# Kernel tuning notes

Hardware: AMD Instinct MI355X
Metric: run time of the kernel (lower is better)

The kernel has to match this reference:

```python
import jax, jax.numpy as jnp
import numpy as np

P, B, I, O = 32, 512, 1024, 1024


def setup_inputs() -> dict:
    key = jax.random.key(0)
    kx, kw = jax.random.split(key)
    # strictly {0,1}-valued binary tensors stored as float32, as in the torch module
    x = (jax.random.uniform(kx, (P, B, I)) > 0.5).astype(jnp.float32)
    w = (jax.random.uniform(kw, (2, P, I, O)) > 0.5).astype(jnp.float32)
    return {"x": x, "w": w}


def reference(x, w):
    # x: [P, B, I] binary; w: [2, P, I, O] binary.
    # out = x @ W0 + (~x) @ W1  (logical_not of a {0,1} float is 1 - x)
    notx = 1.0 - x
    out = jnp.einsum('pbi,pio->pbo', x, w[0]) + jnp.einsum('pbi,pio->pbo', notx, w[1])
    return out  # [P, B, O], activation == 'none'
```

## Files before the change

kernel.cpp:

```cpp
#include <hip/hip_runtime.h>


namespace {

constexpr int PP = 32;
constexpr int BB = 512;
constexpr int II = 1024;
constexpr int OO = 1024;

typedef __attribute__((ext_vector_type(8))) short bf16x8;
typedef __attribute__((ext_vector_type(4))) float f32x4;

__device__ __forceinline__ unsigned pk2(float lo, float hi) {
    return (__float_as_uint(lo) >> 16) | (__float_as_uint(hi) & 0xFFFF0000u);
}

__global__ __launch_bounds__(256, 2) void ebl_prep(const float* __restrict__ x,
                                                   const float* __restrict__ w,
                                                   unsigned short* __restrict__ dWT,
                                                   unsigned short* __restrict__ xbf,
                                                   float* __restrict__ colsum) {
    const int t = (int)threadIdx.x;
    const int bid = (int)blockIdx.x;

    if (bid < 256) {
        const int p  = bid >> 3;
        const int o0 = (bid & 7) * 128;
        const int og = t & 31;
        const int kg = t >> 5;
        const int o  = o0 + 4 * og;
        const float* w0p = w + (size_t)p * (II * OO) + o;
        const float* w1p = w + (size_t)(PP + p) * (II * OO) + o;

        float cs0 = 0.f, cs1 = 0.f, cs2 = 0.f, cs3 = 0.f;

        for (int it = 0; it < 16; ++it) {
            const int kb = 64 * it + 8 * kg;
            const float* r0 = w0p + (size_t)kb * OO;
            const float* r1 = w1p + (size_t)kb * OO;
            f32x4 q0[8], q1[8];
#pragma unroll
            for (int j = 0; j < 8; ++j) q0[j] = *(const f32x4*)(r0 + (size_t)j * OO);
#pragma unroll
            for (int j = 0; j < 8; ++j) q1[j] = *(const f32x4*)(r1 + (size_t)j * OO);

#pragma unroll
            for (int c = 0; c < 4; ++c) {
                uint4 st;
                st.x = pk2(q0[0][c] - q1[0][c], q0[1][c] - q1[1][c]);
                st.y = pk2(q0[2][c] - q1[2][c], q0[3][c] - q1[3][c]);
                st.z = pk2(q0[4][c] - q1[4][c], q0[5][c] - q1[5][c]);
                st.w = pk2(q0[6][c] - q1[6][c], q0[7][c] - q1[7][c]);
                *(uint4*)(&dWT[((size_t)p * OO + o + c) * II + kb]) = st;
            }
#pragma unroll
            for (int j = 0; j < 8; ++j) {
                cs0 += q1[j].x; cs1 += q1[j].y; cs2 += q1[j].z; cs3 += q1[j].w;
            }
        }

        __shared__ float Scr[8 * 128];
        *(f32x4*)(&Scr[kg * 128 + 4 * og]) = (f32x4){cs0, cs1, cs2, cs3};
        __syncthreads();
        if (t < 128) {
            float s = 0.f;
#pragma unroll
            for (int g = 0; g < 8; ++g) s += Scr[g * 128 + t];
            colsum[p * OO + o0 + t] = s;
        }
    } else {
        const size_t base = (size_t)(bid - 256) * 65536;
        for (int it = 0; it < 16; ++it) {
#pragma unroll
            for (int j = 0; j < 4; ++j) {
                const size_t idx = base + (size_t)it * 4096 + j * 1024 + 4 * t;
                f32x4 v = *(const f32x4*)(x + idx);
                *(uint2*)(&xbf[idx]) = make_uint2(pk2(v.x, v.y), pk2(v.z, v.w));
            }
        }
    }
}

__device__ __forceinline__ void load_lds16(const unsigned short* g, unsigned short* l) {
    __builtin_amdgcn_global_load_lds(
        (const __attribute__((address_space(1))) unsigned int*)g,
        (__attribute__((address_space(3))) unsigned int*)l, 16, 0, 0);
}

__global__ __launch_bounds__(256, 3) void ebl_gemm(const unsigned short* __restrict__ xbf,
                                                   const unsigned short* __restrict__ dWT,
                                                   const float* __restrict__ colsum,
                                                   float* __restrict__ out) {
    __shared__ __align__(16) unsigned short As[128 * 64];
    __shared__ __align__(16) unsigned short Bs[128 * 64];

    const int t  = (int)threadIdx.x;
    const int l  = t & 63;
    const int wv = t >> 6;
    const int wm = wv & 1;
    const int wn = wv >> 1;
    const int lq = l >> 4;
    const int ln = l & 15;

    const int p  = (int)blockIdx.z;
    const int b0 = (int)blockIdx.y * 128;
    const int o0 = (int)blockIdx.x * 128;

    const unsigned short* Ag = xbf + ((size_t)p * BB + b0) * II;
    const unsigned short* Bg = dWT + ((size_t)p * OO + o0) * II;

    const int ri = l >> 3, sj = l & 7;
    int gof[4], lbase[4];
#pragma unroll
    for (int q = 0; q < 4; ++q) {
        const int r0  = 8 * (4 * wv + q);
        const int row = r0 + ri;
        gof[q]   = row * II + 8 * (sj ^ (row & 7));
        lbase[q] = r0 * 64;
    }

    int aoff[2][4], boff[2][4];
#pragma unroll
    for (int s = 0; s < 2; ++s)
#pragma unroll
        for (int mt = 0; mt < 4; ++mt) {
            const int j = 8 * ((4 * s + lq) ^ (ln & 7));
            aoff[s][mt] = (wm * 64 + mt * 16 + ln) * 64 + j;
            boff[s][mt] = (wn * 64 + mt * 16 + ln) * 64 + j;
        }

    f32x4 acc[4][4];
#pragma unroll
    for (int mt = 0; mt < 4; ++mt)
#pragma unroll
        for (int nt = 0; nt < 4; ++nt)
            acc[mt][nt] = (f32x4){0.f, 0.f, 0.f, 0.f};

    for (int kk = 0; kk < II; kk += 64) {
#pragma unroll
        for (int q = 0; q < 4; ++q) {
            load_lds16(Ag + gof[q] + kk, As + lbase[q]);
            load_lds16(Bg + gof[q] + kk, Bs + lbase[q]);
        }
        __syncthreads();

#pragma unroll
        for (int s = 0; s < 2; ++s) {
            bf16x8 af[4], bfv[4];
#pragma unroll
            for (int mt = 0; mt < 4; ++mt) af[mt] = *(const bf16x8*)(As + aoff[s][mt]);
#pragma unroll
            for (int nt = 0; nt < 4; ++nt) bfv[nt] = *(const bf16x8*)(Bs + boff[s][nt]);
#pragma unroll
            for (int mt = 0; mt < 4; ++mt)
#pragma unroll
                for (int nt = 0; nt < 4; ++nt)
                    acc[mt][nt] = __builtin_amdgcn_mfma_f32_16x16x32_bf16(
                        af[mt], bfv[nt], acc[mt][nt], 0, 0, 0);
        }
        __syncthreads();
    }

    float cs[4];
#pragma unroll
    for (int nt = 0; nt < 4; ++nt)
        cs[nt] = colsum[p * OO + o0 + wn * 64 + nt * 16 + ln];

    float* op = out + ((size_t)p * BB + b0) * OO + o0;
#pragma unroll
    for (int nt = 0; nt < 4; ++nt) {
        const int ocol = wn * 64 + nt * 16 + ln;
#pragma unroll
        for (int mt = 0; mt < 4; ++mt) {
            const int row = wm * 64 + mt * 16 + lq * 4;
#pragma unroll
            for (int r = 0; r < 4; ++r)
                op[(size_t)(row + r) * OO + ocol] = acc[mt][nt][r] + cs[nt];
        }
    }
}

}

extern "C" void kernel_launch(void* const* d_in, const int* in_sizes, int n_in,
                              void* d_out, int out_size, void* d_ws, size_t ws_size,
                              hipStream_t stream) {
    const float* x = (const float*)d_in[0];
    const float* w = (const float*)d_in[1];
    float* out = (float*)d_out;

    unsigned short* dWT = (unsigned short*)d_ws;
    unsigned short* xbf = (unsigned short*)((char*)d_ws + (64u << 20));
    float* colsum = (float*)((char*)d_ws + (96u << 20));

    ebl_prep<<<dim3(512, 1, 1), dim3(256, 1, 1), 0, stream>>>(x, w, dWT, xbf, colsum);
    ebl_gemm<<<dim3(OO / 128, BB / 128, PP), dim3(256, 1, 1), 0, stream>>>(
        xbf, dWT, colsum, out);
}
```

Baseline: 483.4 us.

## Fuse fp32-to-bf16 conversion and weight differencing into a single GEMM kernel

Replaces the separate prep kernel and bf16 GEMM with one kernel. It DMAs fp32 x, W0 and W1 tiles straight into LDS, converts x to bf16 and builds (W0-W1) in bf16 in LDS, and accumulates the W1 column sums in the same pass. The colsum bias is added through an LDS-staged, vectorized output store. This drops the intermediate workspace writes and the extra launch. In exchange each block re-reads fp32 inputs across tiles (twice the bytes of bf16, redundant across output tiles), uses a smaller per-wave MFMA tile, and adds LDS conversion passes with extra barriers in every k-step.

```diff
diff --git a/kernel.cpp b/kernel.cpp
--- a/kernel.cpp
+++ b/kernel.cpp
@@ -4,7 +4,7 @@
 namespace {
 
 constexpr int PP = 32;
-constexpr int BB = 512;
+constexpr int BBATCH = 512;
 constexpr int II = 1024;
 constexpr int OO = 1024;
 
@@ -15,84 +15,25 @@
     return (__float_as_uint(lo) >> 16) | (__float_as_uint(hi) & 0xFFFF0000u);
 }
 
-__global__ __launch_bounds__(256, 2) void ebl_prep(const float* __restrict__ x,
-                                                   const float* __restrict__ w,
-                                                   unsigned short* __restrict__ dWT,
-                                                   unsigned short* __restrict__ xbf,
-                                                   float* __restrict__ colsum) {
-    const int t = (int)threadIdx.x;
-    const int bid = (int)blockIdx.x;
-
-    if (bid < 256) {
-        const int p  = bid >> 3;
-        const int o0 = (bid & 7) * 128;
-        const int og = t & 31;
-        const int kg = t >> 5;
-        const int o  = o0 + 4 * og;
-        const float* w0p = w + (size_t)p * (II * OO) + o;
-        const float* w1p = w + (size_t)(PP + p) * (II * OO) + o;
-
-        float cs0 = 0.f, cs1 = 0.f, cs2 = 0.f, cs3 = 0.f;
-
-        for (int it = 0; it < 16; ++it) {
-            const int kb = 64 * it + 8 * kg;
-            const float* r0 = w0p + (size_t)kb * OO;
-            const float* r1 = w1p + (size_t)kb * OO;
-            f32x4 q0[8], q1[8];
-#pragma unroll
-            for (int j = 0; j < 8; ++j) q0[j] = *(const f32x4*)(r0 + (size_t)j * OO);
-#pragma unroll
-            for (int j = 0; j < 8; ++j) q1[j] = *(const f32x4*)(r1 + (size_t)j * OO);
-
-#pragma unroll
-            for (int c = 0; c < 4; ++c) {
-                uint4 st;
-                st.x = pk2(q0[0][c] - q1[0][c], q0[1][c] - q1[1][c]);
-                st.y = pk2(q0[2][c] - q1[2][c], q0[3][c] - q1[3][c]);
-                st.z = pk2(q0[4][c] - q1[4][c], q0[5][c] - q1[5][c]);
-                st.w = pk2(q0[6][c] - q1[6][c], q0[7][c] - q1[7][c]);
-                *(uint4*)(&dWT[((size_t)p * OO + o + c) * II + kb]) = st;
-            }
-#pragma unroll
-            for (int j = 0; j < 8; ++j) {
-                cs0 += q1[j].x; cs1 += q1[j].y; cs2 += q1[j].z; cs3 += q1[j].w;
-            }
-        }
-
-        __shared__ float Scr[8 * 128];
-        *(f32x4*)(&Scr[kg * 128 + 4 * og]) = (f32x4){cs0, cs1, cs2, cs3};
-        __syncthreads();
-        if (t < 128) {
-            float s = 0.f;
-#pragma unroll
-            for (int g = 0; g < 8; ++g) s += Scr[g * 128 + t];
-            colsum[p * OO + o0 + t] = s;
-        }
-    } else {
-        const size_t base = (size_t)(bid - 256) * 65536;
-        for (int it = 0; it < 16; ++it) {
-#pragma unroll
-            for (int j = 0; j < 4; ++j) {
-                const size_t idx = base + (size_t)it * 4096 + j * 1024 + 4 * t;
-                f32x4 v = *(const f32x4*)(x + idx);
-                *(uint2*)(&xbf[idx]) = make_uint2(pk2(v.x, v.y), pk2(v.z, v.w));
-            }
-        }
-    }
-}
-
-__device__ __forceinline__ void load_lds16(const unsigned short* g, unsigned short* l) {
+__device__ __forceinline__ void dma16(const float* g, char* l) {
     __builtin_amdgcn_global_load_lds(
         (const __attribute__((address_space(1))) unsigned int*)g,
         (__attribute__((address_space(3))) unsigned int*)l, 16, 0, 0);
 }
 
-__global__ __launch_bounds__(256, 3) void ebl_gemm(const unsigned short* __restrict__ xbf,
-                                                   const unsigned short* __restrict__ dWT,
-                                                   const float* __restrict__ colsum,
-                                                   float* __restrict__ out) {
-    __shared__ __align__(16) unsigned short As[128 * 64];
-    __shared__ __align__(16) unsigned short Bs[128 * 64];
+constexpr int XF   = 0;
+constexpr int W0F  = 16384;
+constexpr int W1F  = 32768;
+constexpr int ABo  = 49152;
+constexpr int BBo  = 59392;
+constexpr int LDST = 69632;
+constexpr int OUTS = 0;
+constexpr int CSP  = 36864;
+
+__global__ __launch_bounds__(512, 4) void ebl_kernel(const float* __restrict__ x,
+                                                     const float* __restrict__ w,
+                                                     float* __restrict__ out) {
+    __shared__ __align__(16) char smem[LDST];
 
     const int t  = (int)threadIdx.x;
     const int l  = t & 63;
@@ -106,76 +47,153 @@
     const int b0 = (int)blockIdx.y * 128;
     const int o0 = (int)blockIdx.x * 128;
 
-    const unsigned short* Ag = xbf + ((size_t)p * BB + b0) * II;
-    const unsigned short* Bg = dWT + ((size_t)p * OO + o0) * II;
-
-    const int ri = l >> 3, sj = l & 7;
-    int gof[4], lbase[4];
-#pragma unroll
-    for (int q = 0; q < 4; ++q) {
-        const int r0  = 8 * (4 * wv + q);
-        const int row = r0 + ri;
-        gof[q]   = row * II + 8 * (sj ^ (row & 7));
-        lbase[q] = r0 * 64;
+    const float* xg  = x + ((size_t)p * BBATCH + b0) * II;
+    const float* w0g = w + (size_t)p * II * OO + o0;
+    const float* w1g = w + (size_t)(PP + p) * II * OO + o0;
+
+    const int xrow_l = (l >> 3);
+    const int xcol_l = (l & 7) * 4;
+    const int wrow_l = (l >> 5);
+    const int wcol_l = (l & 31) * 4;
+
+    int a_off[4], b_off[2];
+#pragma unroll
+    for (int mt = 0; mt < 4; ++mt)
+        a_off[mt] = ABo + (wm * 64 + mt * 16 + ln) * 80 + lq * 16;
+#pragma unroll
+    for (int nt = 0; nt < 2; ++nt)
+        b_off[nt] = BBo + (wn * 32 + nt * 16 + ln) * 80 + lq * 16;
+
+    f32x4 acc[4][2];
+#pragma unroll
+    for (int mt = 0; mt < 4; ++mt)
+#pragma unroll
+        for (int nt = 0; nt < 2; ++nt)
+            acc[mt][nt] = (f32x4){0.f, 0.f, 0.f, 0.f};
+
+    const int cm = t & 31;
+    const int kg = (t >> 5) & 7;
+    const int au = t & 255;
+
+    f32x4 cs = (f32x4){0.f, 0.f, 0.f, 0.f};
+
+    auto dma_step = [&](int kk) {
+        const int kbase = kk * 32;
+        if (wv < 2) {
+#pragma unroll
+            for (int q = 0; q < 8; ++q) {
+                const int r0 = wv * 64 + 8 * q;
+                dma16(xg + (size_t)(r0 + xrow_l) * II + kbase + xcol_l,
+                      smem + XF + r0 * 128);
+            }
+        } else if (wv < 4) {
+#pragma unroll
+            for (int q = 0; q < 8; ++q) {
+                const int kr0 = (wv - 2) * 16 + 2 * q;
+                dma16(w0g + (size_t)(kbase + kr0 + wrow_l) * OO + wcol_l,
+                      smem + W0F + kr0 * 512);
+            }
+        } else if (wv < 6) {
+#pragma unroll
+            for (int q = 0; q < 8; ++q) {
+                const int kr0 = (wv - 4) * 16 + 2 * q;
+                dma16(w1g + (size_t)(kbase + kr0 + wrow_l) * OO + wcol_l,
+                      smem + W1F + kr0 * 512);
+            }
+        }
+    };
+
+    auto convert_step = [&]() {
+        if (t < 256) {
+            f32x4 d[4];
+            f32x4 b1s[4];
+#pragma unroll
+            for (int j = 0; j < 4; ++j) {
+                const int krow = 4 * kg + j;
+                f32x4 a = *(const f32x4*)(smem + W0F + krow * 512 + cm * 16);
+                f32x4 b = *(const f32x4*)(smem + W1F + krow * 512 + cm * 16);
+                d[j] = a - b;
+                b1s[j] = b;
+            }
+            cs += b1s[0]; cs += b1s[1]; cs += b1s[2]; cs += b1s[3];
+#pragma unroll
+            for (int c = 0; c < 4; ++c) {
+                uint2 v = make_uint2(pk2(d[0][c], d[1][c]), pk2(d[2][c], d[3][c]));
+                *(uint2*)(smem + BBo + (4 * cm + c) * 80 + 8 * kg) = v;
+            }
+        } else {
+#pragma unroll
+            for (int s = 0; s < 4; ++s) {
+                const int f = au + 256 * s;
+                const int row = f >> 3, ch = f & 7;
+                f32x4 v = *(const f32x4*)(smem + XF + row * 128 + ch * 16);
+                *(uint2*)(smem + ABo + row * 80 + ch * 8) =
+                    make_uint2(pk2(v.x, v.y), pk2(v.z, v.w));
+            }
+        }
+    };
+
+    auto mfma_step = [&]() {
+        bf16x8 af[4], bf[2];
+#pragma unroll
+        for (int mt = 0; mt < 4; ++mt) af[mt] = *(const bf16x8*)(smem + a_off[mt]);
+#pragma unroll
+        for (int nt = 0; nt < 2; ++nt) bf[nt] = *(const bf16x8*)(smem + b_off[nt]);
+#pragma unroll
+        for (int mt = 0; mt < 4; ++mt)
+#pragma unroll
+            for (int nt = 0; nt < 2; ++nt)
+                acc[mt][nt] = __builtin_amdgcn_mfma_f32_16x16x32_bf16(
+                    af[mt], bf[nt], acc[mt][nt], 0, 0, 0);
+    };
+
+    dma_step(0);
+    __syncthreads();
+    convert_step();
+    __syncthreads();
+
+    for (int kk = 1; kk < 32; ++kk) {
+        dma_step(kk);
+        mfma_step();
+        __syncthreads();
+        convert_step();
+        __syncthreads();
     }
-
-    int aoff[2][4], boff[2][4];
-#pragma unroll
-    for (int s = 0; s < 2; ++s)
-#pragma unroll
-        for (int mt = 0; mt < 4; ++mt) {
-            const int j = 8 * ((4 * s + lq) ^ (ln & 7));
-            aoff[s][mt] = (wm * 64 + mt * 16 + ln) * 64 + j;
-            boff[s][mt] = (wn * 64 + mt * 16 + ln) * 64 + j;
-        }
-
-    f32x4 acc[4][4];
-#pragma unroll
-    for (int mt = 0; mt < 4; ++mt)
-#pragma unroll
-        for (int nt = 0; nt < 4; ++nt)
-            acc[mt][nt] = (f32x4){0.f, 0.f, 0.f, 0.f};
-
-    for (int kk = 0; kk < II; kk += 64) {
-#pragma unroll
-        for (int q = 0; q < 4; ++q) {
-            load_lds16(Ag + gof[q] + kk, As + lbase[q]);
-            load_lds16(Bg + gof[q] + kk, Bs + lbase[q]);
-        }
-        __syncthreads();
-
-#pragma unroll
-        for (int s = 0; s < 2; ++s) {
-            bf16x8 af[4], bfv[4];
-#pragma unroll
-            for (int mt = 0; mt < 4; ++mt) af[mt] = *(const bf16x8*)(As + aoff[s][mt]);
-#pragma unroll
-            for (int nt = 0; nt < 4; ++nt) bfv[nt] = *(const bf16x8*)(Bs + boff[s][nt]);
+    mfma_step();
+
+    if (t < 256)
+        *(f32x4*)(smem + CSP + kg * 512 + cm * 16) = cs;
+    __syncthreads();
+    f32x4 csr = (f32x4){0.f, 0.f, 0.f, 0.f};
+#pragma unroll
+    for (int g = 0; g < 8; ++g)
+        csr += *(const f32x4*)(smem + CSP + g * 512 + (t & 31) * 16);
+
+#pragma unroll
+    for (int h = 0; h < 2; ++h) {
+        __syncthreads();
+        if (wm == h) {
 #pragma unroll
             for (int mt = 0; mt < 4; ++mt)
 #pragma unroll
-                for (int nt = 0; nt < 4; ++nt)
-                    acc[mt][nt] = __builtin_amdgcn_mfma_f32_16x16x32_bf16(
-                        af[mt], bfv[nt], acc[mt][nt], 0, 0, 0);
-        }
-        __syncthreads();
-    }
-
-    float cs[4];
-#pragma unroll
-    for (int nt = 0; nt < 4; ++nt)
-        cs[nt] = colsum[p * OO + o0 + wn * 64 + nt * 16 + ln];
-
-    float* op = out + ((size_t)p * BB + b0) * OO + o0;
-#pragma unroll
-    for (int nt = 0; nt < 4; ++nt) {
-        const int ocol = wn * 64 + nt * 16 + ln;
-#pragma unroll
-        for (int mt = 0; mt < 4; ++mt) {
-            const int row = wm * 64 + mt * 16 + lq * 4;
-#pragma unroll
-            for (int r = 0; r < 4; ++r)
-                op[(size_t)(row + r) * OO + ocol] = acc[mt][nt][r] + cs[nt];
+                for (int nt = 0; nt < 2; ++nt) {
+                    const int col = wn * 32 + nt * 16 + ln;
+#pragma unroll
+                    for (int r = 0; r < 4; ++r) {
+                        const int rl = mt * 16 + lq * 4 + r;
+                        *(float*)(smem + OUTS + rl * 528 + col * 4) = acc[mt][nt][r];
+                    }
+                }
+        }
+        __syncthreads();
+#pragma unroll
+        for (int s = 0; s < 4; ++s) {
+            const int idx = t + 512 * s;
+            const int rl = idx >> 5, c = idx & 31;
+            f32x4 v = *(const f32x4*)(smem + OUTS + rl * 528 + c * 16);
+            v += csr;
+            *(f32x4*)(out + ((size_t)(p * BBATCH + b0 + 64 * h + rl)) * OO + o0 +
+                      4 * c) = v;
         }
     }
 }
@@ -188,12 +206,6 @@
     const float* x = (const float*)d_in[0];
     const float* w = (const float*)d_in[1];
     float* out = (float*)d_out;
-
-    unsigned short* dWT = (unsigned short*)d_ws;
-    unsigned short* xbf = (unsigned short*)((char*)d_ws + (64u << 20));
-    float* colsum = (float*)((char*)d_ws + (96u << 20));
-
-    ebl_prep<<<dim3(512, 1, 1), dim3(256, 1, 1), 0, stream>>>(x, w, dWT, xbf, colsum);
-    ebl_gemm<<<dim3(OO / 128, BB / 128, PP), dim3(256, 1, 1), 0, stream>>>(
-        xbf, dWT, colsum, out);
-}
+    dim3 grid(OO / 128, BBATCH / 128, PP);
+    ebl_kernel<<<grid, dim3(512, 1, 1), 0, stream>>>(x, w, out);
+}
```

Result: slower. 703.7 us (+45.6%).
